# Optimization experiments

Hardware: AMD Instinct MI355X
Metric: run time of the kernel (lower is better)

The kernel has to match this reference:

```python
import jax, jax.numpy as jnp
import numpy as np

ALPHA = 0.2  # LeakyReLU negative slope
N, IN_DIM, OUT_DIM = 8192, 512, 64


def setup_inputs() -> dict:
    key = jax.random.key(0)
    k1, k2, k3, k4 = jax.random.split(key, 4)
    X = jax.random.normal(k1, (N, IN_DIM), dtype=jnp.float32)
    Adj = jax.random.randint(k2, (N, N), 0, 2, dtype=jnp.int32)
    # xavier_uniform with gain=1.414
    def xavier(k, shape, gain=1.414):
        fan_in, fan_out = shape[0], shape[1]
        bound = gain * np.sqrt(6.0 / (fan_in + fan_out))
        return jax.random.uniform(k, shape, jnp.float32, -bound, bound)
    W = xavier(k3, (IN_DIM, OUT_DIM))
    a = xavier(k4, (2 * OUT_DIM, 1))
    return {"X": X, "Adj": Adj, "W": W, "a": a}


def reference(X, Adj, W, a):
    # h = X @ W : [N, D]
    h = X @ W
    D = h.shape[1]
    # Decompose pairwise score: concat([h_i, h_j]) @ a == h_i @ a1 + h_j @ a2
    s1 = h @ a[:D, 0]   # [N] -- contribution of row (destination) node i
    s2 = h @ a[D:, 0]   # [N] -- contribution of column (source) node j
    e = jnp.exp(jax.nn.leaky_relu(s1[:, None] + s2[None, :], negative_slope=ALPHA))  # [N, N]
    e = jnp.where(Adj == 0, jnp.float32(0.0), e)
    attention = e / jnp.sum(e, axis=1, keepdims=True)
    # dropout is a no-op in eval mode (training=False)
    return attention @ h
```

## Files before the change

kernel.cpp:

```cpp
#include <hip/hip_runtime.h>
#include <math.h>


#define NN 8192
#define KIN 512
#define DD 64
#define ALPHA 0.2f

#define WJ 256
#define JSPAN 4096
#define NWIN (JSPAN/WJ)
#define ASTR 260
#define ABUF (16 * ASTR)

using floatx4 = __attribute__((ext_vector_type(4))) float;
using bf16x8  = __attribute__((ext_vector_type(8))) __bf16;

__device__ __forceinline__ void glds16(const int* g, int* l) {
    __builtin_amdgcn_global_load_lds((const __attribute__((address_space(1))) void*)g,
                                     (__attribute__((address_space(3))) void*)l, 16, 0, 0);
}

__global__ __launch_bounds__(256) void k_fused(const float* __restrict__ X,
                                               const float* __restrict__ W,
                                               const float* __restrict__ a,
                                               float* __restrict__ s1,
                                               float* __restrict__ s2,
                                               __bf16* __restrict__ hFrag) {
    __shared__ __align__(16) float smem[3200];
    float* XT = smem;
    float* WL = smem + 32 * 36;
    float* hT = smem;
    const int t = threadIdx.x;
    const int i0 = blockIdx.x * 32;
    const int rb = t >> 5;
    const int db = t & 31;
    float acc[4][2] = {};

    for (int k0 = 0; k0 < KIN; k0 += 32) {
        {
            const int row = t >> 3, kq = t & 7;
            const float4 x4 = *(const float4*)(X + (size_t)(i0 + row) * KIN + k0 + kq * 4);
            XT[(kq * 4 + 0) * 36 + row] = x4.x;
            XT[(kq * 4 + 1) * 36 + row] = x4.y;
            XT[(kq * 4 + 2) * 36 + row] = x4.z;
            XT[(kq * 4 + 3) * 36 + row] = x4.w;
#pragma unroll
            for (int p = 0; p < 2; ++p) {
                const int q = p * 256 + t;
                const int kk = q >> 4, dq = q & 15;
                *(float4*)(WL + kk * 64 + dq * 4) =
                    *(const float4*)(W + (size_t)(k0 + kk) * DD + dq * 4);
            }
        }
        __syncthreads();
#pragma unroll
        for (int k = 0; k < 32; ++k) {
            const float4 xa = *(const float4*)(XT + k * 36 + rb * 4);
            const float2 wb = *(const float2*)(WL + k * 64 + db * 2);
            const float xv[4] = {xa.x, xa.y, xa.z, xa.w};
#pragma unroll
            for (int i = 0; i < 4; ++i) {
                acc[i][0] += xv[i] * wb.x;
                acc[i][1] += xv[i] * wb.y;
            }
        }
        __syncthreads();
    }
#pragma unroll
    for (int i = 0; i < 4; ++i) {
        hT[(rb * 4 + i) * 66 + db * 2 + 0] = acc[i][0];
        hT[(rb * 4 + i) * 66 + db * 2 + 1] = acc[i][1];
    }
    __syncthreads();
    {
        const int r = t >> 3, sub = t & 7;
        float p1 = 0.f, p2 = 0.f;
#pragma unroll
        for (int u = 0; u < 8; ++u) {
            const int d = sub * 8 + u;
            const float v = hT[r * 66 + d];
            p1 += v * a[d];
            p2 += v * a[64 + d];
        }
#pragma unroll
        for (int off = 1; off < 8; off <<= 1) {
            p1 += __shfl_xor(p1, off, 64);
            p2 += __shfl_xor(p2, off, 64);
        }
        if (sub == 0) {
            s1[i0 + r] = p1;
            s2[i0 + r] = p2;
        }
    }
    {
        const int lane = t & 63, dt = t >> 6;
        const int n = lane & 15, q = lane >> 4;
        bf16x8 v;
#pragma unroll
        for (int jj = 0; jj < 8; ++jj)
            v[jj] = (__bf16)hT[(q * 8 + jj) * 66 + dt * 16 + n];
        *(bf16x8*)(hFrag + ((size_t)blockIdx.x * 256 + t) * 8) = v;
    }
}

__global__ __launch_bounds__(256) void k_attn8(const bf16x8* __restrict__ hFrag,
                                               const int* __restrict__ Adj,
                                               const float* __restrict__ s1,
                                               const float* __restrict__ s2,
                                               float* __restrict__ numP,
                                               float* __restrict__ denP) {
    __shared__ int lds_adj[2 * ABUF];
    const int t = threadIdx.x;
    const int wv = t >> 6, lane = t & 63;
    const int n = lane & 15, q = lane >> 4;
    const int i0 = (blockIdx.x >> 1) * 16;
    const int jb0 = (blockIdx.x & 1) * JSPAN;
    const float s1v = s1[i0 + n];

    bf16x8 ones;
#pragma unroll
    for (int u = 0; u < 8; ++u) ones[u] = (__bf16)1.0f;

    floatx4 acc[5] = {};

    auto issue = [&](int w, int buf) {
        const int jg0 = jb0 + w * WJ;
#pragma unroll
        for (int r4 = 0; r4 < 4; ++r4) {
            const int r = wv * 4 + r4;
            const int* gsrc = Adj + (size_t)(i0 + r) * NN + jg0 + lane * 4;
            int* ldst = lds_adj + buf * ABUF + r * ASTR;
            glds16(gsrc, ldst);
        }
    };

    issue(0, 0);
    issue(1, 1);

#pragma unroll 1
    for (int w = 0; w < NWIN; ++w) {
        const int buf = w & 1;
        __syncthreads();
        const int* ldsb = lds_adj + buf * ABUF + n * ASTR;
#pragma unroll
        for (int k2 = 0; k2 < 2; ++k2) {
            const int ks = wv * 2 + k2;
            const int jg = jb0 + w * WJ + ks * 32 + q * 8;
            const float4 z0 = *(const float4*)(s2 + jg);
            const float4 z1 = *(const float4*)(s2 + jg + 4);
            const int4 m0 = *(const int4*)(ldsb + ks * 32 + q * 8);
            const int4 m1 = *(const int4*)(ldsb + ks * 32 + q * 8 + 4);
            const int am[8] = {m0.x, m0.y, m0.z, m0.w, m1.x, m1.y, m1.z, m1.w};
            const float zz[8] = {z0.x, z0.y, z0.z, z0.w, z1.x, z1.y, z1.z, z1.w};
            bf16x8 af;
#pragma unroll
            for (int u = 0; u < 8; ++u) {
                const float s = s1v + zz[u];
                const float l = fmaxf(s, ALPHA * s);
                const float e = am[u] ? __expf(l) : 0.f;
                af[u] = (__bf16)e;
            }
            const bf16x8* hf = hFrag + (size_t)(jg >> 5) * 4 * 64 + lane;
#pragma unroll
            for (int dt = 0; dt < 4; ++dt)
                acc[dt] = __builtin_amdgcn_mfma_f32_16x16x32_bf16(af, hf[dt * 64], acc[dt], 0, 0, 0);
            acc[4] = __builtin_amdgcn_mfma_f32_16x16x32_bf16(af, ones, acc[4], 0, 0, 0);
        }
        __syncthreads();
        if (w + 2 < NWIN) issue(w + 2, buf);
    }

    const size_t base = ((size_t)blockIdx.x * 4 + wv) * 1024;
#pragma unroll
    for (int dt = 0; dt < 4; ++dt)
#pragma unroll
        for (int r = 0; r < 4; ++r)
            numP[base + (size_t)(q * 4 + r) * 64 + dt * 16 + n] = acc[dt][r];

    if (n == 0) {
#pragma unroll
        for (int r = 0; r < 4; ++r)
            denP[((size_t)blockIdx.x * 4 + wv) * 16 + q * 4 + r] = acc[4][r];
    }
}

__global__ __launch_bounds__(256) void k_final(const float* __restrict__ numP,
                                               const float* __restrict__ denP,
                                               float* __restrict__ out) {
    const int idx = blockIdx.x * 256 + threadIdx.x;
    const int i = idx >> 6, d = idx & 63;
    const int itile = i >> 4, r = i & 15;
    float num = 0.f, den = 0.f;
#pragma unroll
    for (int jh = 0; jh < 2; ++jh) {
        const int b = itile * 2 + jh;
#pragma unroll
        for (int wv = 0; wv < 4; ++wv) {
            num += numP[((size_t)b * 4 + wv) * 1024 + (size_t)r * 64 + d];
            den += denP[((size_t)b * 4 + wv) * 16 + r];
        }
    }
    out[idx] = num / den;
}

extern "C" void kernel_launch(void* const* d_in, const int* in_sizes, int n_in,
                              void* d_out, int out_size, void* d_ws, size_t ws_size,
                              hipStream_t stream) {
    const float* X = (const float*)d_in[0];
    const int* Adj = (const int*)d_in[1];
    const float* W = (const float*)d_in[2];
    const float* a = (const float*)d_in[3];
    float* out = (float*)d_out;

    float* ws = (float*)d_ws;
    float* s1 = ws;
    float* s2 = s1 + 8192;
    __bf16* hFrag = (__bf16*)(s2 + 8192);
    float* numP = (float*)(s2 + 8192 + 262144);
    float* denP = numP + 1024 * 4 * 1024;

    k_fused<<<256, 256, 0, stream>>>(X, W, a, s1, s2, hFrag);
    k_attn8<<<1024, 256, 0, stream>>>((const bf16x8*)hFrag, Adj, s1, s2, numP, denP);
    k_final<<<2048, 256, 0, stream>>>(numP, denP, out);
}
```

Baseline: 396.7 us.

## Load adjacency directly into registers and reduce partials in-block

Drops the LDS double-buffered global_load_lds staging of the adjacency tile. Each lane now reads its own adjacency row directly from global memory, and each wave owns a 512-column slice of a 2048-column quarter span. The four waves' partial numerators and denominators are summed in shared memory before a single per-block partial is written, which halves the partial buffer traffic and the work in the final kernel. The grid doubles to 2048 blocks for more parallelism, at the cost of less coalesced direct loads (16 rows at a 32KB stride per wave) and no explicit prefetch pipeline.

New measurement: 407.9 us. +2.8%, slower.

```diff
diff --git a/kernel.cpp b/kernel.cpp
--- a/kernel.cpp
+++ b/kernel.cpp
@@ -7,19 +7,8 @@
 #define DD 64
 #define ALPHA 0.2f
 
-#define WJ 256
-#define JSPAN 4096
-#define NWIN (JSPAN/WJ)
-#define ASTR 260
-#define ABUF (16 * ASTR)
-
 using floatx4 = __attribute__((ext_vector_type(4))) float;
 using bf16x8  = __attribute__((ext_vector_type(8))) __bf16;
-
-__device__ __forceinline__ void glds16(const int* g, int* l) {
-    __builtin_amdgcn_global_load_lds((const __attribute__((address_space(1))) void*)g,
-                                     (__attribute__((address_space(3))) void*)l, 16, 0, 0);
-}
 
 __global__ __launch_bounds__(256) void k_fused(const float* __restrict__ X,
                                                const float* __restrict__ W,
@@ -104,19 +93,21 @@
     }
 }
 
-__global__ __launch_bounds__(256) void k_attn8(const bf16x8* __restrict__ hFrag,
-                                               const int* __restrict__ Adj,
-                                               const float* __restrict__ s1,
-                                               const float* __restrict__ s2,
-                                               float* __restrict__ numP,
-                                               float* __restrict__ denP) {
-    __shared__ int lds_adj[2 * ABUF];
+__global__ __launch_bounds__(256) void k_attn_d(const bf16x8* __restrict__ hFrag,
+                                                const int* __restrict__ Adj,
+                                                const float* __restrict__ s1,
+                                                const float* __restrict__ s2,
+                                                float* __restrict__ numP,
+                                                float* __restrict__ denP) {
+    __shared__ float redN[4 * 16 * 66];
+    __shared__ float redD[4 * 16];
     const int t = threadIdx.x;
     const int wv = t >> 6, lane = t & 63;
     const int n = lane & 15, q = lane >> 4;
-    const int i0 = (blockIdx.x >> 1) * 16;
-    const int jb0 = (blockIdx.x & 1) * JSPAN;
+    const int i0 = (blockIdx.x >> 2) * 16;
+    const int jb0 = (blockIdx.x & 3) * 2048 + wv * 512;
     const float s1v = s1[i0 + n];
+    const int* __restrict__ arow = Adj + (size_t)(i0 + n) * NN;
 
     bf16x8 ones;
 #pragma unroll
@@ -124,64 +115,55 @@
 
     floatx4 acc[5] = {};
 
-    auto issue = [&](int w, int buf) {
-        const int jg0 = jb0 + w * WJ;
-#pragma unroll
-        for (int r4 = 0; r4 < 4; ++r4) {
-            const int r = wv * 4 + r4;
-            const int* gsrc = Adj + (size_t)(i0 + r) * NN + jg0 + lane * 4;
-            int* ldst = lds_adj + buf * ABUF + r * ASTR;
-            glds16(gsrc, ldst);
-        }
-    };
-
-    issue(0, 0);
-    issue(1, 1);
-
-#pragma unroll 1
-    for (int w = 0; w < NWIN; ++w) {
-        const int buf = w & 1;
-        __syncthreads();
-        const int* ldsb = lds_adj + buf * ABUF + n * ASTR;
-#pragma unroll
-        for (int k2 = 0; k2 < 2; ++k2) {
-            const int ks = wv * 2 + k2;
-            const int jg = jb0 + w * WJ + ks * 32 + q * 8;
-            const float4 z0 = *(const float4*)(s2 + jg);
-            const float4 z1 = *(const float4*)(s2 + jg + 4);
-            const int4 m0 = *(const int4*)(ldsb + ks * 32 + q * 8);
-            const int4 m1 = *(const int4*)(ldsb + ks * 32 + q * 8 + 4);
-            const int am[8] = {m0.x, m0.y, m0.z, m0.w, m1.x, m1.y, m1.z, m1.w};
-            const float zz[8] = {z0.x, z0.y, z0.z, z0.w, z1.x, z1.y, z1.z, z1.w};
-            bf16x8 af;
-#pragma unroll
-            for (int u = 0; u < 8; ++u) {
-                const float s = s1v + zz[u];
-                const float l = fmaxf(s, ALPHA * s);
-                const float e = am[u] ? __expf(l) : 0.f;
-                af[u] = (__bf16)e;
-            }
-            const bf16x8* hf = hFrag + (size_t)(jg >> 5) * 4 * 64 + lane;
-#pragma unroll
-            for (int dt = 0; dt < 4; ++dt)
-                acc[dt] = __builtin_amdgcn_mfma_f32_16x16x32_bf16(af, hf[dt * 64], acc[dt], 0, 0, 0);
-            acc[4] = __builtin_amdgcn_mfma_f32_16x16x32_bf16(af, ones, acc[4], 0, 0, 0);
-        }
-        __syncthreads();
-        if (w + 2 < NWIN) issue(w + 2, buf);
-    }
-
-    const size_t base = ((size_t)blockIdx.x * 4 + wv) * 1024;
+#pragma unroll 2
+    for (int ks = 0; ks < 16; ++ks) {
+        const int jg = jb0 + ks * 32 + q * 8;
+        const int4 m0 = *(const int4*)(arow + jg);
+        const int4 m1 = *(const int4*)(arow + jg + 4);
+        const float4 z0 = *(const float4*)(s2 + jg);
+        const float4 z1 = *(const float4*)(s2 + jg + 4);
+        const int am[8] = {m0.x, m0.y, m0.z, m0.w, m1.x, m1.y, m1.z, m1.w};
+        const float zz[8] = {z0.x, z0.y, z0.z, z0.w, z1.x, z1.y, z1.z, z1.w};
+        bf16x8 af;
+#pragma unroll
+        for (int u = 0; u < 8; ++u) {
+            const float s = s1v + zz[u];
+            const float l = fmaxf(s, ALPHA * s);
+            const float e = am[u] ? __expf(l) : 0.f;
+            af[u] = (__bf16)e;
+        }
+        const bf16x8* hf = hFrag + (size_t)(jg >> 5) * 256 + lane;
+#pragma unroll
+        for (int dt = 0; dt < 4; ++dt)
+            acc[dt] = __builtin_amdgcn_mfma_f32_16x16x32_bf16(af, hf[dt * 64], acc[dt], 0, 0, 0);
+        acc[4] = __builtin_amdgcn_mfma_f32_16x16x32_bf16(af, ones, acc[4], 0, 0, 0);
+    }
+
 #pragma unroll
     for (int dt = 0; dt < 4; ++dt)
 #pragma unroll
         for (int r = 0; r < 4; ++r)
-            numP[base + (size_t)(q * 4 + r) * 64 + dt * 16 + n] = acc[dt][r];
-
+            redN[wv * 1056 + (q * 4 + r) * 66 + dt * 16 + n] = acc[dt][r];
     if (n == 0) {
 #pragma unroll
         for (int r = 0; r < 4; ++r)
-            denP[((size_t)blockIdx.x * 4 + wv) * 16 + q * 4 + r] = acc[4][r];
+            redD[wv * 16 + q * 4 + r] = acc[4][r];
+    }
+    __syncthreads();
+#pragma unroll
+    for (int k = 0; k < 4; ++k) {
+        const int idx = k * 256 + t;
+        const int r = idx >> 6, d = idx & 63;
+        float num = 0.f;
+#pragma unroll
+        for (int w = 0; w < 4; ++w) num += redN[w * 1056 + r * 66 + d];
+        numP[(size_t)blockIdx.x * 1024 + idx] = num;
+    }
+    if (t < 16) {
+        float den = 0.f;
+#pragma unroll
+        for (int w = 0; w < 4; ++w) den += redD[w * 16 + t];
+        denP[(size_t)blockIdx.x * 16 + t] = den;
     }
 }
 
@@ -190,16 +172,13 @@
                                                float* __restrict__ out) {
     const int idx = blockIdx.x * 256 + threadIdx.x;
     const int i = idx >> 6, d = idx & 63;
-    const int itile = i >> 4, r = i & 15;
+    const int it = i >> 4, r = i & 15;
     float num = 0.f, den = 0.f;
 #pragma unroll
-    for (int jh = 0; jh < 2; ++jh) {
-        const int b = itile * 2 + jh;
-#pragma unroll
-        for (int wv = 0; wv < 4; ++wv) {
-            num += numP[((size_t)b * 4 + wv) * 1024 + (size_t)r * 64 + d];
-            den += denP[((size_t)b * 4 + wv) * 16 + r];
-        }
+    for (int jq = 0; jq < 4; ++jq) {
+        const size_t b = (size_t)(it * 4 + jq);
+        num += numP[b * 1024 + (size_t)r * 64 + d];
+        den += denP[b * 16 + r];
     }
     out[idx] = num / den;
 }
@@ -218,9 +197,9 @@
     float* s2 = s1 + 8192;
     __bf16* hFrag = (__bf16*)(s2 + 8192);
     float* numP = (float*)(s2 + 8192 + 262144);
-    float* denP = numP + 1024 * 4 * 1024;
+    float* denP = numP + 2048 * 1024;
 
     k_fused<<<256, 256, 0, stream>>>(X, W, a, s1, s2, hFrag);
-    k_attn8<<<1024, 256, 0, stream>>>((const bf16x8*)hFrag, Adj, s1, s2, numP, denP);
+    k_attn_d<<<2048, 256, 0, stream>>>((const bf16x8*)hFrag, Adj, s1, s2, numP, denP);
     k_final<<<2048, 256, 0, stream>>>(numP, denP, out);
 }
```
